# Kernel tuning notes

Measured on AMD Instinct MI355X. Metric: run time of the kernel, lower is better.

Reference implementation:

```python
import jax, jax.numpy as jnp
import numpy as np

B, S, E, H = 2, 2048, 1024, 16
Dh = E // H
LN_EPS = 1e-5


def setup_inputs() -> dict:
    key = jax.random.key(0)
    ks = jax.random.split(key, 12)
    std = 1.0 / np.sqrt(E)
    inp = {
        "query": jax.random.normal(ks[0], (B, S, E), jnp.float32),
        "key":   jax.random.normal(ks[1], (B, S, E), jnp.float32),
        "value": jax.random.normal(ks[2], (B, S, E), jnp.float32),
        # True = masked. Causal mask so every row keeps >=1 valid entry.
        "mask": jnp.broadcast_to(jnp.triu(jnp.ones((S, S), bool), k=1), (B, S, S)),
        # per-head QKV projections, stacked: weight [H, Dh, E] (torch Linear layout), bias [H, Dh]
        "Wq_w": jax.random.uniform(ks[3], (H, Dh, E), jnp.float32, -std, std),
        "Wq_b": jax.random.uniform(ks[4], (H, Dh), jnp.float32, -std, std),
        "Wk_w": jax.random.uniform(ks[5], (H, Dh, E), jnp.float32, -std, std),
        "Wk_b": jax.random.uniform(ks[6], (H, Dh), jnp.float32, -std, std),
        "Wv_w": jax.random.uniform(ks[7], (H, Dh, E), jnp.float32, -std, std),
        "Wv_b": jax.random.uniform(ks[8], (H, Dh), jnp.float32, -std, std),
        # output projection [E, E] (torch layout: out = x @ W.T + b)
        "out_w": jax.random.uniform(ks[9], (E, E), jnp.float32, -std, std),
        "out_b": jax.random.uniform(ks[10], (E,), jnp.float32, -std, std),
        "ln_g": jnp.ones((E,), jnp.float32),
        "ln_b": jnp.zeros((E,), jnp.float32),
    }
    return inp


def reference(query, key, value, mask, Wq_w, Wq_b, Wk_w, Wk_b, Wv_w, Wv_b, out_w, out_b, ln_g, ln_b):
    # per-head projections (batched over heads): [B,S,E] x [H,Dh,E] -> [B,H,S,Dh]
    q = jnp.einsum('bse,hde->bhsd', query, Wq_w) + Wq_b[None, :, None, :]
    k = jnp.einsum('bse,hde->bhsd', key,   Wk_w) + Wk_b[None, :, None, :]
    v = jnp.einsum('bse,hde->bhsd', value, Wv_w) + Wv_b[None, :, None, :]
    scale = 1.0 / np.sqrt(Dh).astype(np.float32)
    scores = jnp.einsum('bhsd,bhtd->bhst', q, k) * scale  # [B,H,S,S]
    scores = jnp.where(mask[:, None, :, :], -jnp.inf, scores)
    probs = jax.nn.softmax(scores, axis=-1)  # dropout p=0 (eval)
    ctx = jnp.einsum('bhst,bhtd->bhsd', probs, v)  # [B,H,S,Dh]
    att = ctx.transpose(0, 2, 1, 3).reshape(query.shape[0], query.shape[1], -1)  # concat heads [B,S,E]
    proj = att @ out_w.T + out_b  # dropout p=0
    x = query + proj  # residual
    mu = jnp.mean(x, axis=-1, keepdims=True)
    var = jnp.mean(jnp.square(x - mu), axis=-1, keepdims=True)
    return (x - mu) * jax.lax.rsqrt(var + LN_EPS) * ln_g + ln_b
```

## Files before the change

### kernel.cpp

```cpp
#include <hip/hip_runtime.h>
#include <stdint.h>

#define B_ 2
#define S_ 2048
#define E_ 1024
#define H_ 16
#define DH 64
#define M_TOT (B_*S_)

typedef short s16x8 __attribute__((ext_vector_type(8)));
typedef float f32x4 __attribute__((ext_vector_type(4)));
typedef unsigned int u32;
typedef unsigned short u16;

union V8 { uint4 u; s16x8 v; };

__device__ __forceinline__ u32 fbits(float f){ union{float f;u32 i;}x; x.f=f; return x.i; }
__device__ __forceinline__ u32 prround(float f){ return fbits(f)+0x8000u; }
__device__ __forceinline__ u16 f2bf(float f){ return (u16)(prround(f)>>16); }
__device__ __forceinline__ u32 permpack(u32 hi,u32 lo){ return __builtin_amdgcn_perm(hi,lo,0x07060302u); }
__device__ __forceinline__ uint4 pack8r(const float4 a, const float4 b){
    uint4 p;
    p.x = permpack(prround(a.y),prround(a.x));
    p.y = permpack(prround(a.w),prround(a.z));
    p.z = permpack(prround(b.y),prround(b.x));
    p.w = permpack(prround(b.w),prround(b.z));
    return p;
}
__device__ __forceinline__ float exp2_fast(float x){ float r; asm("v_exp_f32 %0, %1":"=v"(r):"v"(x)); return r; }

typedef const __attribute__((address_space(1))) u32* gas_t;
typedef __attribute__((address_space(3))) u32* las_t;
#define GLDS16(gp, lp) __builtin_amdgcn_global_load_lds((gas_t)(gp), (las_t)(lp), 16, 0, 0)

__global__ __launch_bounds__(256) void cvtw(
    const float* __restrict__ w0, const float* __restrict__ w1, const float* __restrict__ w2,
    u16* __restrict__ dst, int n4)
{
    const int z = blockIdx.y;
    const float* s = (z==0)?w0:(z==1)?w1:w2;
    u16* d = dst + (size_t)z*E_*E_;
    int i = blockIdx.x*256 + threadIdx.x;
    const int stride = gridDim.x*256;
    for (; i<n4; i+=stride){
        float4 v = ((const float4*)s)[i];
        uint2 p;
        p.x = permpack(prround(v.y),prround(v.x));
        p.y = permpack(prround(v.w),prround(v.z));
        ((uint2*)d)[i] = p;
    }
}
__global__ __launch_bounds__(256) void cvt1(
    const float* __restrict__ s, u16* __restrict__ d, int n4)
{
    int i = blockIdx.x*256 + threadIdx.x;
    const int stride = gridDim.x*256;
    for (; i<n4; i+=stride){
        float4 v = ((const float4*)s)[i];
        uint2 p;
        p.x = permpack(prround(v.y),prround(v.x));
        p.y = permpack(prround(v.w),prround(v.z));
        ((uint2*)d)[i] = p;
    }
}

__global__ __launch_bounds__(256,3) void qkv128(
    const float* __restrict__ xq, const float* __restrict__ xk, const float* __restrict__ xv,
    const u16* __restrict__ Wb,
    const float* __restrict__ bq, const float* __restrict__ bk, const float* __restrict__ bv,
    u16* __restrict__ oq, u16* __restrict__ ok_, u16* __restrict__ ovt)
{
    const int bid = blockIdx.x;
    const int c = bid & 7;
    const int t = bid >> 3;
    const int n = t & 7;
    const int g = ((t >> 3) << 3) + c;
    const int m = g & 31, z = g >> 5;

    const float* X = (z==0)?xq:(z==1)?xk:xv;
    const u16* W = Wb + (size_t)z*E_*E_;
    const float* bia = (z==0)?bq:(z==1)?bk:bv;
    const float scale = (z==0)? 0.125f*1.44269504f : 1.0f;

    __shared__ __align__(16) u16 AsAll[3*128*32];
    __shared__ __align__(16) u16 BsAll[3*128*32];

    const int tid = threadIdx.x;
    const int wid = tid>>6, lane = tid&63;
    const int lrow = lane&15, quad = lane>>4;
    const int mb = m*128, nb = n*128;
    const int wm = (wid>>1)*64, wn = (wid&1)*64;
    const int srow = lane>>2, skq = lane&3;
    const int arow = wid*32 + (lane>>1);
    const int akh  = lane&1;

    f32x4 acc[4][4] = {};
    const float* Xb = X + (size_t)mb*E_;
    const u16*  Wn = W + (size_t)nb*E_;
    const float* Xrow = Xb + (size_t)arow*E_ + akh*16;

    float4 ar[4];
    auto issueA = [&](int k0){
#pragma unroll
        for (int i=0;i<4;i++) ar[i] = *(const float4*)(Xrow + k0 + i*4);
    };
    auto writeA = [&](u16* Ad){
        const int g0 = akh*2;
        const int sw = arow&3;
        const uint4 w0 = pack8r(ar[0], ar[1]);
        const uint4 w1 = pack8r(ar[2], ar[3]);
        *(uint4*)&Ad[arow*32 + ((g0  )^sw)*8] = w0;
        *(uint4*)&Ad[arow*32 + ((g0+1)^sw)*8] = w1;
    };
    auto stageB = [&](u16* Bd, int k0){
#pragma unroll
        for (int i=0;i<2;i++){
            const int rb = wid*32 + i*16;
            GLDS16(Wn + (size_t)(rb+srow)*E_ + k0 + ((skq^(srow&3))<<3), Bd + rb*32);
        }
    };
    auto compute = [&](const u16* Ad, const u16* Bd){
        s16x8 af[4], bfr[4];
        const int sw = lrow&3;
#pragma unroll
        for (int mi=0;mi<4;mi++)
            af[mi] = *(const s16x8*)&Ad[(wm+mi*16+lrow)*32 + (quad^sw)*8];
#pragma unroll
        for (int ci=0;ci<4;ci++)
            bfr[ci] = *(const s16x8*)&Bd[(wn+ci*16+lrow)*32 + (quad^sw)*8];
#pragma unroll
        for (int mi=0;mi<4;mi++)
#pragma unroll
            for (int ci=0;ci<4;ci++)
                acc[mi][ci] = __builtin_amdgcn_mfma_f32_16x16x32_bf16(af[mi], bfr[ci], acc[mi][ci],0,0,0);
    };

    issueA(0);
    stageB(BsAll, 0);
    writeA(AsAll);

    int cur = 0, nxt = 1;
    for (int it=0; it<32; ++it){
        u16* Ac = AsAll + cur*(128*32);
        u16* Bc = BsAll + cur*(128*32);
        u16* An = AsAll + nxt*(128*32);
        u16* Bn = BsAll + nxt*(128*32);
        __syncthreads();
        if (it+1 < 32){
            issueA((it+1)*32);
            stageB(Bn, (it+1)*32);
        }
        compute(Ac, Bc);
        if (it+1 < 32) writeA(An);
        cur = nxt;
        nxt = nxt+1; if (nxt==3) nxt=0;
    }

    if (z < 2){
        u16* O = (z==0)?oq:ok_;
#pragma unroll
        for (int ci=0;ci<4;ci++){
            const int nn = nb+wn+ci*16+lrow;
            const float bval = bia[nn];
            const int h = nn>>6, d = nn&63;
#pragma unroll
            for (int mi=0;mi<4;mi++){
#pragma unroll
                for (int r=0;r<4;r++){
                    const int mm = mb+wm+mi*16+quad*4+r;
                    const int bb = mm>>11, s = mm&(S_-1);
                    O[(((size_t)(bb*H_+h))*S_+s)*DH + d] = f2bf((acc[mi][ci][r]+bval)*scale);
                }
            }
        }
    } else {
#pragma unroll
        for (int ci=0;ci<4;ci++){
            const int nn = nb+wn+ci*16+lrow;
            const float bval = bia[nn];
            const int h = nn>>6, d = nn&63;
#pragma unroll
            for (int mi=0;mi<4;mi++){
                const int m0 = mb+wm+mi*16+quad*4;
                const int bb = m0>>11, s0 = m0&(S_-1);
                uint2 pk;
                pk.x = permpack(prround(acc[mi][ci][1]+bval), prround(acc[mi][ci][0]+bval));
                pk.y = permpack(prround(acc[mi][ci][3]+bval), prround(acc[mi][ci][2]+bval));
                *(uint2*)&ovt[(((size_t)(bb*H_+h))*DH + d)*S_ + s0] = pk;
            }
        }
    }
}

__global__ __launch_bounds__(256) void attn(
    const u16* __restrict__ q_ws, const u16* __restrict__ k_ws,
    const u16* __restrict__ vt_ws, u16* __restrict__ att)
{
    const int bid = blockIdx.x;
    const int c8 = bid & 7;
    const int t = bid >> 3;
    const int p = t & 15;
    const int bh = ((t >> 4) << 3) + c8;
    const int b = bh>>4, h = bh&15;

    const u16* Qb = q_ws + (size_t)bh*S_*DH;
    const u16* Kb = k_ws + (size_t)bh*S_*DH;
    const u16* VT = vt_ws + (size_t)bh*DH*S_;

    __shared__ __align__(16) u16 Ks0[64*64];
    __shared__ __align__(16) u16 Ks1[64*64];
    __shared__ __align__(16) u16 Vt0[64*64];
    __shared__ __align__(16) u16 Vt1[64*64];
    __shared__ __align__(16) u16 Ps[4][16*64];

    const int tid = threadIdx.x;
    const int wid = tid>>6, lane = tid&63;
    const int lrow = lane&15, quad = lane>>4;
    u16* Pw = Ps[wid];

    const int srw = lane>>3;
    const int scs = lane&7;
    const int sgc = scs ^ srw;

    auto stageKV = [&](u16* Kd, u16* Vd, int t0){
#pragma unroll
        for (int g2=0; g2<2; g2++){
            const int rg = wid*16 + g2*8 + srw;
            GLDS16(Kb + (size_t)(t0+rg)*DH + (sgc<<3), Kd + (wid*16+g2*8)*64);
            GLDS16(VT + (size_t)rg*S_ + t0 + (sgc<<3), Vd + (wid*16+g2*8)*64);
        }
    };

    for (int ph=0; ph<2; ph++){
        const int qi = ph ? (31-p) : p;
        const int qb = qi<<6;

        s16x8 qf[2];
#pragma unroll
        for (int ch=0;ch<2;ch++)
            qf[ch] = *(const s16x8*)&Qb[(size_t)(qb+wid*16+lrow)*DH + ch*32 + quad*8];

        f32x4 o[4] = {};
        float l_lane = 0.f;
        const int qglob = qb + wid*16 + lrow;
        const int ntile = qi + 1;

        auto computeTile = [&](const u16* Kd, const u16* Vd, int t0, bool diag){
            f32x4 st[4] = {};
#pragma unroll
            for (int tt=0;tt<4;tt++){
                const int tr = tt*16+lrow;
#pragma unroll
                for (int ch=0;ch<2;ch++){
                    const int slot = (ch*4+quad) ^ (lrow&7);
                    const s16x8 kf = *(const s16x8*)&Kd[tr*64 + slot*8];
                    st[tt] = __builtin_amdgcn_mfma_f32_16x16x32_bf16(kf, qf[ch], st[tt],0,0,0);
                }
            }
            if (diag){
#pragma unroll
                for (int tt=0;tt<4;tt++){
                    const int tg = t0 + tt*16 + quad*4;
#pragma unroll
                    for (int r=0;r<4;r++)
                        if (tg + r > qglob) st[tt][r] = -1e30f;
                }
            }
#pragma unroll
            for (int tt=0;tt<4;tt++){
                const float p0 = exp2_fast(st[tt][0]);
                const float p1 = exp2_fast(st[tt][1]);
                const float p2 = exp2_fast(st[tt][2]);
                const float p3 = exp2_fast(st[tt][3]);
                l_lane += (p0+p1)+(p2+p3);
                const int tc = tt*2 + (quad>>1);
                const int ts = tc ^ (lrow&7);
                const int a0 = lrow*64 + ts*8 + (quad&1)*4;
                *(u32*)&Pw[a0]   = permpack(prround(p1),prround(p0));
                *(u32*)&Pw[a0+2] = permpack(prround(p3),prround(p2));
            }
            s16x8 pb[2];
#pragma unroll
            for (int ch=0;ch<2;ch++){
                const int slot = (ch*4+quad) ^ (lrow&7);
                pb[ch] = *(const s16x8*)&Pw[lrow*64 + slot*8];
            }
#pragma unroll
            for (int cc=0;cc<4;cc++){
                const int vr = cc*16+lrow;
#pragma unroll
                for (int ch=0;ch<2;ch++){
                    const int slot = (ch*4+quad) ^ (lrow&7);
                    const s16x8 vf = *(const s16x8*)&Vd[vr*64 + slot*8];
                    o[cc] = __builtin_amdgcn_mfma_f32_16x16x32_bf16(vf, pb[ch], o[cc],0,0,0);
                }
            }
        };

        __syncthreads();
        stageKV(Ks0, Vt0, 0);
        for (int ti=0; ; ti+=2){
            __syncthreads();
            if (ti+1 < ntile) stageKV(Ks1, Vt1, (ti+1)<<6);
            computeTile(Ks0, Vt0, ti<<6, ti==ntile-1);
            if (ti+1 >= ntile) break;
            __syncthreads();
            if (ti+2 < ntile) stageKV(Ks0, Vt0, (ti+2)<<6);
            computeTile(Ks1, Vt1, (ti+1)<<6, ti+1==ntile-1);
            if (ti+2 >= ntile) break;
        }

        float s = l_lane;
        s += __shfl_xor(s, 16, 64);
        s += __shfl_xor(s, 32, 64);
        const float rl = 1.0f/s;

#pragma unroll
        for (int cc=0;cc<4;cc++){
            uint2 pk;
            pk.x = permpack(prround(o[cc][1]*rl), prround(o[cc][0]*rl));
            pk.y = permpack(prround(o[cc][3]*rl), prround(o[cc][2]*rl));
            *(uint2*)&att[(size_t)(b*S_ + qglob)*E_ + h*DH + cc*16 + quad*4] = pk;
        }
    }
}

__global__ __launch_bounds__(256) void oproj128(
    const u16* __restrict__ A, const u16* __restrict__ W, const float* __restrict__ bias,
    const float* __restrict__ resid, float* __restrict__ out)
{
    const int bid = blockIdx.x;
    const int c = bid & 7;
    const int t = bid >> 3;
    const int n = t & 15;
    const int m = ((t >> 4) << 3) + c;

    __shared__ __align__(16) u16 As0[128*32];
    __shared__ __align__(16) u16 As1[128*32];
    __shared__ __align__(16) u16 Bs0[64*32];
    __shared__ __align__(16) u16 Bs1[64*32];

    const int tid = threadIdx.x;
    const int wid = tid>>6, lane = tid&63;
    const int lrow = lane&15, quad = lane>>4;
    const int mb = m*128, nb = n*64;
    const int srow = lane>>2, skq = lane&3;

    f32x4 acc[2][4] = {};
    const u16* Ab = A + (size_t)mb*E_;
    const u16* Wn = W + (size_t)nb*E_;

    auto stage = [&](u16* Ad, u16* Bd, int k0){
        const int kc = (skq^(srow&3))<<3;
#pragma unroll
        for (int i=0;i<2;i++){
            const int rb = wid*32 + i*16;
            GLDS16(Ab + (size_t)(rb+srow)*E_ + k0 + kc, Ad + rb*32);
        }
        GLDS16(Wn + (size_t)(wid*16+srow)*E_ + k0 + kc, Bd + (wid*16)*32);
    };
    auto compute = [&](const u16* Ad, const u16* Bd){
        s16x8 af[2], bfr[4];
        const int sw = lrow&3;
#pragma unroll
        for (int mi=0;mi<2;mi++)
            af[mi] = *(const s16x8*)&Ad[(wid*32+mi*16+lrow)*32 + (quad^sw)*8];
#pragma unroll
        for (int ci=0;ci<4;ci++)
            bfr[ci] = *(const s16x8*)&Bd[(ci*16+lrow)*32 + (quad^sw)*8];
#pragma unroll
        for (int mi=0;mi<2;mi++)
#pragma unroll
            for (int ci=0;ci<4;ci++)
                acc[mi][ci] = __builtin_amdgcn_mfma_f32_16x16x32_bf16(af[mi], bfr[ci], acc[mi][ci],0,0,0);
    };

    stage(As0, Bs0, 0);
    for (int k0=0; k0<E_; k0+=64){
        __syncthreads();
        if (k0+32 < E_) stage(As1, Bs1, k0+32);
        compute(As0, Bs0);
        __syncthreads();
        if (k0+64 < E_) stage(As0, Bs0, k0+64);
        compute(As1, Bs1);
    }

#pragma unroll
    for (int ci=0;ci<4;ci++){
        const int nn = nb+ci*16+lrow;
        const float bval = bias[nn];
#pragma unroll
        for (int mi=0;mi<2;mi++){
#pragma unroll
            for (int r=0;r<4;r++){
                const int mm = mb+wid*32+mi*16+quad*4+r;
                out[(size_t)mm*E_+nn] = acc[mi][ci][r] + bval + resid[(size_t)mm*E_+nn];
            }
        }
    }
}

__global__ __launch_bounds__(256) void ln_k(
    const float* __restrict__ xin, const float* __restrict__ lg,
    const float* __restrict__ lb, float* __restrict__ out)
{
    const int row = blockIdx.x;
    const int tid = threadIdx.x;
    const int wid = tid>>6, lane = tid&63;
    const float* xr = xin + (size_t)row*E_;

    float x[4];
    float s = 0.f;
#pragma unroll
    for (int i=0;i<4;i++){ const int e = i*256+tid; x[i] = xr[e]; s += x[i]; }
    __shared__ float red[8];
#pragma unroll
    for (int off=32; off>0; off>>=1) s += __shfl_xor(s, off, 64);
    if (lane==0) red[wid] = s;
    __syncthreads();
    const float mu = (red[0]+red[1]+red[2]+red[3]) * (1.f/E_);

    float v = 0.f;
#pragma unroll
    for (int i=0;i<4;i++){ const float d = x[i]-mu; v += d*d; }
#pragma unroll
    for (int off=32; off>0; off>>=1) v += __shfl_xor(v, off, 64);
    if (lane==0) red[wid+4] = v;
    __syncthreads();
    const float var = (red[4]+red[5]+red[6]+red[7]) * (1.f/E_);
    const float rs = rsqrtf(var + 1e-5f);

#pragma unroll
    for (int i=0;i<4;i++){
        const int e = i*256+tid;
        out[(size_t)row*E_+e] = (x[i]-mu)*rs*lg[e] + lb[e];
    }
}

extern "C" void kernel_launch(void* const* d_in, const int* in_sizes, int n_in,
                              void* d_out, int out_size, void* d_ws, size_t ws_size,
                              hipStream_t stream) {
    const float* q_in = (const float*)d_in[0];
    const float* k_in = (const float*)d_in[1];
    const float* v_in = (const float*)d_in[2];
    const float* wq = (const float*)d_in[4];
    const float* bq = (const float*)d_in[5];
    const float* wk = (const float*)d_in[6];
    const float* bk = (const float*)d_in[7];
    const float* wv = (const float*)d_in[8];
    const float* bv = (const float*)d_in[9];
    const float* ow = (const float*)d_in[10];
    const float* ob = (const float*)d_in[11];
    const float* lg = (const float*)d_in[12];
    const float* lb = (const float*)d_in[13];
    float* out = (float*)d_out;

    char* ws = (char*)d_ws;
    const size_t MB = (size_t)1<<20;
    u16* q_ws  = (u16*)(ws);
    u16* k_ws  = (u16*)(ws +  8*MB);
    u16* vt_ws = (u16*)(ws + 16*MB);
    u16* att   = (u16*)(ws + 24*MB);
    u16* Wbf   = (u16*)(ws + 24*MB);
    u16* owbf  = (u16*)(ws + 16*MB);
    float* proj = (float*)ws;

    cvtw<<<dim3(512,3), 256, 0, stream>>>(wq, wk, wv, Wbf, (E_*E_)/4);
    qkv128<<<dim3(768), 256, 0, stream>>>(
        q_in, k_in, v_in, Wbf, bq, bk, bv, q_ws, k_ws, vt_ws);
    attn<<<dim3(512), 256, 0, stream>>>(q_ws, k_ws, vt_ws, att);
    cvt1<<<dim3(1024), 256, 0, stream>>>(ow, owbf, (E_*E_)/4);
    oproj128<<<dim3(512), 256, 0, stream>>>(att, owbf, ob, q_in, proj);
    ln_k<<<dim3(M_TOT), 256, 0, stream>>>(proj, lg, lb, out);
}
```

Before: 258.2 us.

## Deepen QKV and out-projection GEMM pipelines to three stages with hand-placed waits

Both projection GEMMs now prefetch two K tiles ahead into a 3-slot LDS ring. A single manual s_waitcnt plus a raw s_barrier replaces the __syncthreads pairs, so only the next tile's loads stay in flight. The MFMA sequence is unrolled by hand, with the LDS fragment reads and A-tile conversion interleaved between MFMA groups under s_setprio. The aim is to hide global and LDS latency behind the matrix ops. In exchange, oproj uses more LDS and correctness depends on the hand-counted vmcnt values.

```diff
diff --git a/kernel.cpp b/kernel.cpp
--- a/kernel.cpp
+++ b/kernel.cpp
@@ -32,6 +32,8 @@
 typedef const __attribute__((address_space(1))) u32* gas_t;
 typedef __attribute__((address_space(3))) u32* las_t;
 #define GLDS16(gp, lp) __builtin_amdgcn_global_load_lds((gas_t)(gp), (las_t)(lp), 16, 0, 0)
+
+#define MFMA16(a,b,c) __builtin_amdgcn_mfma_f32_16x16x32_bf16((a),(b),(c),0,0,0)
 
 __global__ __launch_bounds__(256) void cvtw(
     const float* __restrict__ w0, const float* __restrict__ w1, const float* __restrict__ w2,
@@ -72,9 +74,9 @@
 {
     const int bid = blockIdx.x;
     const int c = bid & 7;
-    const int t = bid >> 3;
-    const int n = t & 7;
-    const int g = ((t >> 3) << 3) + c;
+    const int tdec = bid >> 3;
+    const int n = tdec & 7;
+    const int g = ((tdec >> 3) << 3) + c;
     const int m = g & 31, z = g >> 5;
 
     const float* X = (z==0)?xq:(z==1)?xk:xv;
@@ -82,8 +84,8 @@
     const float* bia = (z==0)?bq:(z==1)?bk:bv;
     const float scale = (z==0)? 0.125f*1.44269504f : 1.0f;
 
-    __shared__ __align__(16) u16 AsAll[3*128*32];
-    __shared__ __align__(16) u16 BsAll[3*128*32];
+    __shared__ __align__(16) u16 As[3][128*32];
+    __shared__ __align__(16) u16 Bs[3][128*32];
 
     const int tid = threadIdx.x;
     const int wid = tid>>6, lane = tid&63;
@@ -100,7 +102,8 @@
     const float* Xrow = Xb + (size_t)arow*E_ + akh*16;
 
     float4 ar[4];
-    auto issueA = [&](int k0){
+    auto issueA = [&](int kt){
+        const int k0 = kt*32;
 #pragma unroll
         for (int i=0;i<4;i++) ar[i] = *(const float4*)(Xrow + k0 + i*4);
     };
@@ -109,52 +112,67 @@
         const int sw = arow&3;
         const uint4 w0 = pack8r(ar[0], ar[1]);
         const uint4 w1 = pack8r(ar[2], ar[3]);
-        *(uint4*)&Ad[arow*32 + ((g0  )^sw)*8] = w0;
-        *(uint4*)&Ad[arow*32 + ((g0+1)^sw)*8] = w1;
+        *(uint4*)&Ad[arow*32 + (((g0  )^sw)<<3)] = w0;
+        *(uint4*)&Ad[arow*32 + (((g0+1)^sw)<<3)] = w1;
     };
-    auto stageB = [&](u16* Bd, int k0){
+    auto stageB = [&](u16* Bd, int kt){
+        const int k0 = kt*32;
 #pragma unroll
         for (int i=0;i<2;i++){
             const int rb = wid*32 + i*16;
             GLDS16(Wn + (size_t)(rb+srow)*E_ + k0 + ((skq^(srow&3))<<3), Bd + rb*32);
         }
     };
-    auto compute = [&](const u16* Ad, const u16* Bd){
-        s16x8 af[4], bfr[4];
+
+    issueA(0); stageB(Bs[0], 0); writeA(As[0]);
+    issueA(1); stageB(Bs[1], 1); writeA(As[1]);
+
+    int tc = 0, tn = 2;
+    for (int kt=0; kt<32; ++kt){
+        const int ts = (kt+2 < 32) ? kt+2 : 31;
+        asm volatile("s_waitcnt vmcnt(2) lgkmcnt(0)" ::: "memory");
+        __builtin_amdgcn_s_barrier();
+        __builtin_amdgcn_sched_barrier(0);
+
+        const u16* Ad = As[tc];
+        const u16* Bd = Bs[tc];
         const int sw = lrow&3;
-#pragma unroll
-        for (int mi=0;mi<4;mi++)
-            af[mi] = *(const s16x8*)&Ad[(wm+mi*16+lrow)*32 + (quad^sw)*8];
-#pragma unroll
-        for (int ci=0;ci<4;ci++)
-            bfr[ci] = *(const s16x8*)&Bd[(wn+ci*16+lrow)*32 + (quad^sw)*8];
-#pragma unroll
-        for (int mi=0;mi<4;mi++)
-#pragma unroll
-            for (int ci=0;ci<4;ci++)
-                acc[mi][ci] = __builtin_amdgcn_mfma_f32_16x16x32_bf16(af[mi], bfr[ci], acc[mi][ci],0,0,0);
-    };
-
-    issueA(0);
-    stageB(BsAll, 0);
-    writeA(AsAll);
-
-    int cur = 0, nxt = 1;
-    for (int it=0; it<32; ++it){
-        u16* Ac = AsAll + cur*(128*32);
-        u16* Bc = BsAll + cur*(128*32);
-        u16* An = AsAll + nxt*(128*32);
-        u16* Bn = BsAll + nxt*(128*32);
-        __syncthreads();
-        if (it+1 < 32){
-            issueA((it+1)*32);
-            stageB(Bn, (it+1)*32);
-        }
-        compute(Ac, Bc);
-        if (it+1 < 32) writeA(An);
-        cur = nxt;
-        nxt = nxt+1; if (nxt==3) nxt=0;
-    }
+        s16x8 a0 = *(const s16x8*)&Ad[(wm+ 0+lrow)*32 + ((quad^sw)<<3)];
+        s16x8 a1 = *(const s16x8*)&Ad[(wm+16+lrow)*32 + ((quad^sw)<<3)];
+        s16x8 b0 = *(const s16x8*)&Bd[(wn+ 0+lrow)*32 + ((quad^sw)<<3)];
+        s16x8 b1 = *(const s16x8*)&Bd[(wn+16+lrow)*32 + ((quad^sw)<<3)];
+        s16x8 b2 = *(const s16x8*)&Bd[(wn+32+lrow)*32 + ((quad^sw)<<3)];
+        s16x8 b3 = *(const s16x8*)&Bd[(wn+48+lrow)*32 + ((quad^sw)<<3)];
+        issueA(ts);
+        __builtin_amdgcn_sched_barrier(0);
+        stageB(Bs[tn], ts);
+        __builtin_amdgcn_s_setprio(1);
+        acc[0][0] = MFMA16(a0, b0, acc[0][0]);
+        acc[0][1] = MFMA16(a0, b1, acc[0][1]);
+        acc[0][2] = MFMA16(a0, b2, acc[0][2]);
+        acc[0][3] = MFMA16(a0, b3, acc[0][3]);
+        acc[1][0] = MFMA16(a1, b0, acc[1][0]);
+        acc[1][1] = MFMA16(a1, b1, acc[1][1]);
+        acc[1][2] = MFMA16(a1, b2, acc[1][2]);
+        acc[1][3] = MFMA16(a1, b3, acc[1][3]);
+        __builtin_amdgcn_s_setprio(0);
+        s16x8 a2 = *(const s16x8*)&Ad[(wm+32+lrow)*32 + ((quad^sw)<<3)];
+        s16x8 a3 = *(const s16x8*)&Ad[(wm+48+lrow)*32 + ((quad^sw)<<3)];
+        writeA(As[tn]);
+        __builtin_amdgcn_s_setprio(1);
+        acc[2][0] = MFMA16(a2, b0, acc[2][0]);
+        acc[2][1] = MFMA16(a2, b1, acc[2][1]);
+        acc[2][2] = MFMA16(a2, b2, acc[2][2]);
+        acc[2][3] = MFMA16(a2, b3, acc[2][3]);
+        acc[3][0] = MFMA16(a3, b0, acc[3][0]);
+        acc[3][1] = MFMA16(a3, b1, acc[3][1]);
+        acc[3][2] = MFMA16(a3, b2, acc[3][2]);
+        acc[3][3] = MFMA16(a3, b3, acc[3][3]);
+        __builtin_amdgcn_s_setprio(0);
+        tc = (tc+1==3)?0:tc+1;
+        tn = (tn+1==3)?0:tn+1;
+    }
+    asm volatile("s_waitcnt vmcnt(0)" ::: "memory");
 
     if (z < 2){
         u16* O = (z==0)?oq:ok_;
@@ -331,14 +349,12 @@
 {
     const int bid = blockIdx.x;
     const int c = bid & 7;
-    const int t = bid >> 3;
-    const int n = t & 15;
-    const int m = ((t >> 4) << 3) + c;
-
-    __shared__ __align__(16) u16 As0[128*32];
-    __shared__ __align__(16) u16 As1[128*32];
-    __shared__ __align__(16) u16 Bs0[64*32];
-    __shared__ __align__(16) u16 Bs1[64*32];
+    const int tdec = bid >> 3;
+    const int n = tdec & 15;
+    const int m = ((tdec >> 4) << 3) + c;
+
+    __shared__ __align__(16) u16 As[3][128*32];
+    __shared__ __align__(16) u16 Bs[3][64*32];
 
     const int tid = threadIdx.x;
     const int wid = tid>>6, lane = tid&63;
@@ -350,7 +366,8 @@
     const u16* Ab = A + (size_t)mb*E_;
     const u16* Wn = W + (size_t)nb*E_;
 
-    auto stage = [&](u16* Ad, u16* Bd, int k0){
+    auto stage = [&](u16* Ad, u16* Bd, int kt){
+        const int k0 = kt*32;
         const int kc = (skq^(srow&3))<<3;
 #pragma unroll
         for (int i=0;i<2;i++){
@@ -359,31 +376,41 @@
         }
         GLDS16(Wn + (size_t)(wid*16+srow)*E_ + k0 + kc, Bd + (wid*16)*32);
     };
-    auto compute = [&](const u16* Ad, const u16* Bd){
-        s16x8 af[2], bfr[4];
+
+    stage(As[0], Bs[0], 0);
+    stage(As[1], Bs[1], 1);
+
+    int tc = 0, tn = 2;
+    for (int kt=0; kt<32; ++kt){
+        const int ts = (kt+2 < 32) ? kt+2 : 31;
+        asm volatile("s_waitcnt vmcnt(3) lgkmcnt(0)" ::: "memory");
+        __builtin_amdgcn_s_barrier();
+        __builtin_amdgcn_sched_barrier(0);
+
+        const u16* Ad = As[tc];
+        const u16* Bd = Bs[tc];
         const int sw = lrow&3;
-#pragma unroll
-        for (int mi=0;mi<2;mi++)
-            af[mi] = *(const s16x8*)&Ad[(wid*32+mi*16+lrow)*32 + (quad^sw)*8];
-#pragma unroll
-        for (int ci=0;ci<4;ci++)
-            bfr[ci] = *(const s16x8*)&Bd[(ci*16+lrow)*32 + (quad^sw)*8];
-#pragma unroll
-        for (int mi=0;mi<2;mi++)
-#pragma unroll
-            for (int ci=0;ci<4;ci++)
-                acc[mi][ci] = __builtin_amdgcn_mfma_f32_16x16x32_bf16(af[mi], bfr[ci], acc[mi][ci],0,0,0);
-    };
-
-    stage(As0, Bs0, 0);
-    for (int k0=0; k0<E_; k0+=64){
-        __syncthreads();
-        if (k0+32 < E_) stage(As1, Bs1, k0+32);
-        compute(As0, Bs0);
-        __syncthreads();
-        if (k0+64 < E_) stage(As0, Bs0, k0+64);
-        compute(As1, Bs1);
-    }
+        s16x8 a0 = *(const s16x8*)&Ad[(wid*32+ 0+lrow)*32 + ((quad^sw)<<3)];
+        s16x8 a1 = *(const s16x8*)&Ad[(wid*32+16+lrow)*32 + ((quad^sw)<<3)];
+        s16x8 b0 = *(const s16x8*)&Bd[( 0+lrow)*32 + ((quad^sw)<<3)];
+        s16x8 b1 = *(const s16x8*)&Bd[(16+lrow)*32 + ((quad^sw)<<3)];
+        s16x8 b2 = *(const s16x8*)&Bd[(32+lrow)*32 + ((quad^sw)<<3)];
+        s16x8 b3 = *(const s16x8*)&Bd[(48+lrow)*32 + ((quad^sw)<<3)];
+        stage(As[tn], Bs[tn], ts);
+        __builtin_amdgcn_s_setprio(1);
+        acc[0][0] = MFMA16(a0, b0, acc[0][0]);
+        acc[0][1] = MFMA16(a0, b1, acc[0][1]);
+        acc[0][2] = MFMA16(a0, b2, acc[0][2]);
+        acc[0][3] = MFMA16(a0, b3, acc[0][3]);
+        acc[1][0] = MFMA16(a1, b0, acc[1][0]);
+        acc[1][1] = MFMA16(a1, b1, acc[1][1]);
+        acc[1][2] = MFMA16(a1, b2, acc[1][2]);
+        acc[1][3] = MFMA16(a1, b3, acc[1][3]);
+        __builtin_amdgcn_s_setprio(0);
+        tc = (tc+1==3)?0:tc+1;
+        tn = (tn+1==3)?0:tn+1;
+    }
+    asm volatile("s_waitcnt vmcnt(0)" ::: "memory");
 
 #pragma unroll
     for (int ci=0;ci<4;ci++){
```

After: 253.7 us. No clear change (-1.7%).
